# Optimization experiments

Hardware: AMD Instinct MI355X
Metric: run time of the kernel (lower is better)

## Reference

```python
import jax, jax.numpy as jnp
import numpy as np

D_MODEL = 1024
NUM_HEADS = 16
HEAD_DIM = D_MODEL // NUM_HEADS  # d_k = d_v = 64


def setup_inputs() -> dict:
    key = jax.random.key(0)
    ks = jax.random.split(key, 11)
    B, S = 2, 2048
    s = 1.0 / np.sqrt(D_MODEL)
    inp = {
        "query": jax.random.normal(ks[0], (B, S, D_MODEL), jnp.float32),
        "key": jax.random.normal(ks[1], (B, S, D_MODEL), jnp.float32),
        "value": jax.random.normal(ks[2], (B, S, D_MODEL), jnp.float32),
        "Wq": jax.random.normal(ks[3], (D_MODEL, D_MODEL), jnp.float32) * s,
        "bq": jax.random.normal(ks[4], (D_MODEL,), jnp.float32) * s,
        "Wk": jax.random.normal(ks[5], (D_MODEL, D_MODEL), jnp.float32) * s,
        "bk": jax.random.normal(ks[6], (D_MODEL,), jnp.float32) * s,
        "Wv": jax.random.normal(ks[7], (D_MODEL, D_MODEL), jnp.float32) * s,
        "bv": jax.random.normal(ks[8], (D_MODEL,), jnp.float32) * s,
        "Wo": jax.random.normal(ks[9], (D_MODEL, D_MODEL), jnp.float32) * s,
        "bo": jax.random.normal(ks[10], (D_MODEL,), jnp.float32) * s,
    }
    return inp


def reference(query, key, value, Wq, bq, Wk, bk, Wv, bv, Wo, bo):
    B, Sq, _ = query.shape
    # Linear projections (torch Linear: x @ W.T + b), split into heads
    def proj(x, W, b):
        y = x @ W.T + b  # [B, S, d_model]
        return y.reshape(B, -1, NUM_HEADS, HEAD_DIM).transpose(0, 2, 1, 3)  # [B, H, S, d]

    Q = proj(query, Wq, bq)
    K = proj(key, Wk, bk)
    V = proj(value, Wv, bv)

    scale = 1.0 / jnp.sqrt(jnp.asarray(HEAD_DIM, Q.dtype))
    scores = jnp.einsum("bhqd,bhkd->bhqk", Q, K) * scale  # [B, H, Sq, Sk]
    attn = jax.nn.softmax(scores, axis=-1)
    out = jnp.einsum("bhqk,bhkd->bhqd", attn, V)  # [B, H, Sq, d]
    out = out.transpose(0, 2, 1, 3).reshape(B, Sq, NUM_HEADS * HEAD_DIM)
    return out @ Wo.T + bo
```

## Files before the change

### kernel.cpp

```cpp
#include <hip/hip_runtime.h>
#include <hip/hip_bf16.h>

#define D_MODEL 1024
#define NHEADS  16
#define HDIM    64
#define BATCH   2
#define SEQ     2048
#define MTOT    (BATCH*SEQ)

typedef __attribute__((ext_vector_type(8))) short bf16x8;
typedef __attribute__((ext_vector_type(4))) float f32x4;

__device__ __forceinline__ void async_load16(const void* g, void* l) {
    __builtin_amdgcn_global_load_lds(
        (const __attribute__((address_space(1))) void*)g,
        (__attribute__((address_space(3))) void*)l, 16, 0, 0);
}

__device__ __forceinline__ short f2b(float x) {
    __hip_bfloat16 h = __float2bfloat16(x);
    return *reinterpret_cast<short*>(&h);
}
__device__ __forceinline__ unsigned pack2(float lo, float hi) {
    return (unsigned)(unsigned short)f2b(lo) | ((unsigned)(unsigned short)f2b(hi) << 16);
}

__global__ void cvt_all(const float* __restrict__ s0, const float* __restrict__ s1,
                        const float* __restrict__ s2, const float* __restrict__ s3,
                        const float* __restrict__ s4, const float* __restrict__ s5,
                        const float* __restrict__ s6,
                        short* __restrict__ d0, short* __restrict__ d1,
                        short* __restrict__ d2, short* __restrict__ d3,
                        short* __restrict__ d4, short* __restrict__ d5,
                        short* __restrict__ d6) {
    int bx = blockIdx.x;
    const float* src; short* dst; int blk;
    if (bx < 6144) {
        int t = bx >> 11; blk = bx & 2047;
        src = t == 0 ? s0 : (t == 1 ? s1 : s2);
        dst = t == 0 ? d0 : (t == 1 ? d1 : d2);
    } else {
        int t = (bx - 6144) >> 9; blk = (bx - 6144) & 511;
        src = t == 0 ? s3 : (t == 1 ? s4 : (t == 2 ? s5 : s6));
        dst = t == 0 ? d3 : (t == 1 ? d4 : (t == 2 ? d5 : d6));
    }
    int i = (blk * 256 + threadIdx.x) * 8;
    const float4* s4p = (const float4*)(src + i);
    float4 a = s4p[0], b = s4p[1];
    bf16x8 o;
    o[0]=f2b(a.x); o[1]=f2b(a.y); o[2]=f2b(a.z); o[3]=f2b(a.w);
    o[4]=f2b(b.x); o[5]=f2b(b.y); o[6]=f2b(b.z); o[7]=f2b(b.w);
    *(bf16x8*)(dst + i) = o;
}

__device__ __forceinline__ void gemm_core(const short* __restrict__ A,
                                          const short* __restrict__ Bt,
                                          int K, int m0, int n0,
                                          f32x4 (&acc)[4][4]) {
    __shared__ short As[128 * 32];
    __shared__ short Bs[128 * 32];
    const int lane = threadIdx.x & 63;
    const int wid  = threadIdx.x >> 6;
    const int wm   = (wid >> 1) * 64;
    const int wn   = (wid & 1) * 64;
    const int q    = lane & 15;
    const int quad = lane >> 4;
    const int lr   = lane >> 2;
    const int swzs = (lr + (lr >> 2)) & 3;
    const int cA   = (((lane & 3) ^ swzs)) * 8;
    const int kg   = (quad ^ ((q + (q >> 2)) & 3)) * 8;

#pragma unroll
    for (int mi = 0; mi < 4; mi++)
#pragma unroll
        for (int ni = 0; ni < 4; ni++)
            acc[mi][ni] = f32x4{0.f, 0.f, 0.f, 0.f};

    for (int k0 = 0; k0 < K; k0 += 32) {
#pragma unroll
        for (int c = 0; c < 2; ++c) {
            int chunk = wid * 2 + c;
            const short* ga = A  + (size_t)(m0 + chunk * 16 + lr) * K + k0 + cA;
            async_load16(ga, (char*)As + chunk * 1024);
            const short* gb = Bt + (size_t)(n0 + chunk * 16 + lr) * K + k0 + cA;
            async_load16(gb, (char*)Bs + chunk * 1024);
        }
        __syncthreads();
        bf16x8 af[4], bfr[4];
#pragma unroll
        for (int mi = 0; mi < 4; mi++)
            af[mi] = *(const bf16x8*)&As[(wm + mi * 16 + q) * 32 + kg];
#pragma unroll
        for (int ni = 0; ni < 4; ni++)
            bfr[ni] = *(const bf16x8*)&Bs[(wn + ni * 16 + q) * 32 + kg];
#pragma unroll
        for (int mi = 0; mi < 4; mi++)
#pragma unroll
            for (int ni = 0; ni < 4; ni++)
                acc[mi][ni] = __builtin_amdgcn_mfma_f32_16x16x32_bf16(
                    af[mi], bfr[ni], acc[mi][ni], 0, 0, 0);
        __syncthreads();
    }
}

#define QSCALE (0.125f * 1.44269504f)
__global__ __launch_bounds__(256) void proj_qkv(
    const short* __restrict__ xq, const short* __restrict__ xk, const short* __restrict__ xv,
    const short* __restrict__ wq, const short* __restrict__ wk, const short* __restrict__ wv,
    const float* __restrict__ bq, const float* __restrict__ bk, const float* __restrict__ bv,
    short* __restrict__ Qo, short* __restrict__ Ko, short* __restrict__ Vo) {
    const int z = blockIdx.z;
    const short* A    = z == 0 ? xq : (z == 1 ? xk : xv);
    const short* Bt   = z == 0 ? wq : (z == 1 ? wk : wv);
    const float* bias = z == 0 ? bq : (z == 1 ? bk : bv);
    short*       Out  = z == 0 ? Qo : (z == 1 ? Ko : Vo);
    const float scale = (z == 0) ? QSCALE : 1.0f;

    const int m0 = blockIdx.y * 128, n0 = blockIdx.x * 128;
    f32x4 acc[4][4];
    gemm_core(A, Bt, D_MODEL, m0, n0, acc);

    const int lane = threadIdx.x & 63;
    const int wid  = threadIdx.x >> 6;
    const int q = lane & 15, quad = lane >> 4;
    const int wm = (wid >> 1) * 64, wn = (wid & 1) * 64;
#pragma unroll
    for (int mi = 0; mi < 4; mi++)
#pragma unroll
        for (int ni = 0; ni < 4; ni++)
#pragma unroll
            for (int r = 0; r < 4; r++) {
                int m = m0 + wm + mi * 16 + quad * 4 + r;
                int n = n0 + wn + ni * 16 + q;
                float v = (acc[mi][ni][r] + bias[n]) * scale;
                int b = m >> 11, s = m & (SEQ - 1);
                int h = n >> 6, d = n & 63;
                Out[((size_t)(b * NHEADS + h) * SEQ + s) * HDIM + d] = f2b(v);
            }
}

__global__ __launch_bounds__(256) void gemm_out(
    const short* __restrict__ O, const short* __restrict__ wo,
    const float* __restrict__ bo, float* __restrict__ out) {
    const int m0 = blockIdx.y * 128, n0 = blockIdx.x * 128;
    f32x4 acc[4][4];
    gemm_core(O, wo, D_MODEL, m0, n0, acc);

    const int lane = threadIdx.x & 63;
    const int wid  = threadIdx.x >> 6;
    const int wm = (wid >> 1) * 64, wn = (wid & 1) * 64;
#pragma unroll
    for (int mi = 0; mi < 4; mi++)
#pragma unroll
        for (int ni = 0; ni < 4; ni++)
#pragma unroll
            for (int r = 0; r < 4; r++) {
                int m = m0 + wm + mi * 16 + (lane >> 4) * 4 + r;
                int n = n0 + wn + ni * 16 + (lane & 15);
                out[(size_t)m * D_MODEL + n] = acc[mi][ni][r] + bo[n];
            }
}

__global__ __launch_bounds__(256) void transpose_v(const short* __restrict__ Vp,
                                                   short* __restrict__ Vt) {
    const int bh = blockIdx.y, ts = blockIdx.x;
    __shared__ short T[64][72];
    const int tid = threadIdx.x;
    const int r = tid >> 2, c = (tid & 3) * 16;
    const bf16x8* g = (const bf16x8*)(Vp + ((size_t)bh * SEQ + ts * 64 + r) * HDIM + c);
    *(bf16x8*)&T[r][c]     = g[0];
    *(bf16x8*)&T[r][c + 8] = g[1];
    __syncthreads();
    bf16x8 o0, o1;
#pragma unroll
    for (int j = 0; j < 8; j++) o0[j] = T[c + j][r];
#pragma unroll
    for (int j = 0; j < 8; j++) o1[j] = T[c + 8 + j][r];
    short* dst = Vt + ((size_t)bh * HDIM + r) * SEQ + ts * 64 + c;
    *(bf16x8*)dst = o0;
    *(bf16x8*)(dst + 8) = o1;
}

#define C2 24.0f
__global__ __launch_bounds__(256, 2) void attn(
    const short* __restrict__ Q, const short* __restrict__ K,
    const short* __restrict__ Vt, short* __restrict__ O) {
    const int n = blockIdx.x;
    const int bh = ((n >> 8) << 3) | (n & 7);
    const int qb = (n >> 3) & 31;
    const int b = bh >> 4, h = bh & 15;
    const int q0 = qb * 64;
    const int lane = threadIdx.x & 63;
    const int w = threadIdx.x >> 6;
    const int q = lane & 15, quad = lane >> 4;
    const short* Qb  = Q + (size_t)bh * SEQ * HDIM;
    const short* Kb  = K + (size_t)bh * SEQ * HDIM;
    const short* Vtb = Vt + (size_t)bh * HDIM * SEQ;

    bf16x8 qf[4][2];
#pragma unroll
    for (int g = 0; g < 4; ++g)
#pragma unroll
        for (int c = 0; c < 2; ++c)
            qf[g][c] = *(const bf16x8*)(Qb + (size_t)(q0 + g * 16 + q) * HDIM +
                                        c * 32 + quad * 8);

    float lpart[4] = {0.f, 0.f, 0.f, 0.f};
    f32x4 oacc[4][4];
#pragma unroll
    for (int g = 0; g < 4; ++g)
#pragma unroll
        for (int dt = 0; dt < 4; dt++) oacc[g][dt] = f32x4{0.f, 0.f, 0.f, 0.f};

    const int s0l = ((quad & 1) << 5) | q;
    const int s1l = s0l + 16;

    for (int kt = w; kt < SEQ / 64; kt += 4) {
        const short* Kt = Kb + (size_t)kt * 64 * HDIM;
        bf16x8 kf[2][4], vf[2][4];
#pragma unroll
        for (int t = 0; t < 4; t++)
#pragma unroll
            for (int c = 0; c < 2; ++c)
                kf[c][t] = *(const bf16x8*)(Kt + (size_t)(t * 16 + q) * HDIM +
                                            c * 32 + quad * 8);
#pragma unroll
        for (int dt = 0; dt < 4; dt++)
#pragma unroll
            for (int c = 0; c < 2; ++c)
                vf[c][dt] = *(const bf16x8*)(Vtb + (size_t)(dt * 16 + q) * SEQ +
                                             kt * 64 + c * 32 + quad * 8);

#pragma unroll
        for (int g = 0; g < 4; ++g) {
            f32x4 st[4];
#pragma unroll
            for (int t = 0; t < 4; t++) {
                f32x4 s = f32x4{0.f, 0.f, 0.f, 0.f};
                s = __builtin_amdgcn_mfma_f32_16x16x32_bf16(kf[0][t], qf[g][0], s, 0, 0, 0);
                s = __builtin_amdgcn_mfma_f32_16x16x32_bf16(kf[1][t], qf[g][1], s, 0, 0, 0);
                st[t] = s;
            }
            float lp = lpart[g];
#pragma unroll
            for (int t = 0; t < 4; t++)
#pragma unroll
                for (int r = 0; r < 4; r++) {
                    float p = __builtin_amdgcn_exp2f(st[t][r] - C2);
                    st[t][r] = p;
                    lp += p;
                }
            lpart[g] = lp;
            unsigned pk[4][2];
#pragma unroll
            for (int t = 0; t < 4; t++) {
                pk[t][0] = pack2(st[t][0], st[t][1]);
                pk[t][1] = pack2(st[t][2], st[t][3]);
            }
            bf16x8 pb[2];
#pragma unroll
            for (int c = 0; c < 2; ++c) {
                unsigned lo0 = __shfl(pk[2 * c][0], s0l);
                unsigned lo1 = __shfl(pk[2 * c][1], s0l);
                unsigned lo2 = __shfl(pk[2 * c][0], s1l);
                unsigned lo3 = __shfl(pk[2 * c][1], s1l);
                unsigned hi0 = __shfl(pk[2 * c + 1][0], s0l);
                unsigned hi1 = __shfl(pk[2 * c + 1][1], s0l);
                unsigned hi2 = __shfl(pk[2 * c + 1][0], s1l);
                unsigned hi3 = __shfl(pk[2 * c + 1][1], s1l);
                uint4 u;
                u.x = quad < 2 ? lo0 : hi0;
                u.y = quad < 2 ? lo1 : hi1;
                u.z = quad < 2 ? lo2 : hi2;
                u.w = quad < 2 ? lo3 : hi3;
                pb[c] = __builtin_bit_cast(bf16x8, u);
            }
#pragma unroll
            for (int dt = 0; dt < 4; dt++) {
                oacc[g][dt] = __builtin_amdgcn_mfma_f32_16x16x32_bf16(vf[0][dt], pb[0],
                                                                     oacc[g][dt], 0, 0, 0);
                oacc[g][dt] = __builtin_amdgcn_mfma_f32_16x16x32_bf16(vf[1][dt], pb[1],
                                                                     oacc[g][dt], 0, 0, 0);
            }
        }
    }

    __shared__ f32x4 redO[4][4][64];
    __shared__ float redL[4][64];
#pragma unroll
    for (int g = 0; g < 4; ++g) {
        __syncthreads();
        redL[w][lane] = lpart[g];
#pragma unroll
        for (int dt = 0; dt < 4; dt++) redO[w][dt][lane] = oacc[g][dt];
        __syncthreads();
        float lt = 0.f;
#pragma unroll
        for (int w2 = 0; w2 < 4; ++w2)
#pragma unroll
            for (int qd = 0; qd < 4; ++qd) lt += redL[w2][qd * 16 + q];
        f32x4 o = redO[0][w][lane];
#pragma unroll
        for (int w2 = 1; w2 < 4; ++w2) {
            f32x4 t = redO[w2][w][lane];
#pragma unroll
            for (int r = 0; r < 4; r++) o[r] += t[r];
        }
        const float inv = 1.f / lt;
        const int qg = q0 + g * 16 + q;
        short* orow = O + ((size_t)(b * SEQ + qg)) * D_MODEL + h * HDIM;
        short4 s4;
        s4.x = f2b(o[0] * inv);
        s4.y = f2b(o[1] * inv);
        s4.z = f2b(o[2] * inv);
        s4.w = f2b(o[3] * inv);
        *(short4*)(orow + w * 16 + quad * 4) = s4;
    }
}

extern "C" void kernel_launch(void* const* d_in, const int* in_sizes, int n_in,
                              void* d_out, int out_size, void* d_ws, size_t ws_size,
                              hipStream_t stream) {
    (void)in_sizes; (void)n_in; (void)out_size; (void)ws_size;
    const float* q_in = (const float*)d_in[0];
    const float* k_in = (const float*)d_in[1];
    const float* v_in = (const float*)d_in[2];
    const float* Wq   = (const float*)d_in[3];
    const float* bq   = (const float*)d_in[4];
    const float* Wk   = (const float*)d_in[5];
    const float* bk   = (const float*)d_in[6];
    const float* Wv   = (const float*)d_in[7];
    const float* bv   = (const float*)d_in[8];
    const float* Wo   = (const float*)d_in[9];
    const float* bo   = (const float*)d_in[10];
    float* out = (float*)d_out;

    constexpr size_t MB = 1ull << 20;
    char* ws = (char*)d_ws;
    short* xq  = (short*)(ws + 0 * MB);
    short* xk  = (short*)(ws + 8 * MB);
    short* xv  = (short*)(ws + 16 * MB);
    short* wqb = (short*)(ws + 24 * MB);
    short* wkb = (short*)(ws + 26 * MB);
    short* wvb = (short*)(ws + 28 * MB);
    short* wob = (short*)(ws + 30 * MB);
    short* Qp  = (short*)(ws + 32 * MB);
    short* Kp  = (short*)(ws + 40 * MB);
    short* Vp  = (short*)(ws + 48 * MB);
    short* Op  = (short*)(ws + 56 * MB);
    short* VtG = (short*)(ws + 0 * MB);

    cvt_all<<<8192, 256, 0, stream>>>(q_in, k_in, v_in, Wq, Wk, Wv, Wo,
                                      xq, xk, xv, wqb, wkb, wvb, wob);
    proj_qkv<<<dim3(8, 32, 3), 256, 0, stream>>>(xq, xk, xv, wqb, wkb, wvb,
                                                 bq, bk, bv, Qp, Kp, Vp);
    transpose_v<<<dim3(SEQ / 64, BATCH * NHEADS), 256, 0, stream>>>(Vp, VtG);
    attn<<<1024, 256, 0, stream>>>(Qp, Kp, VtG, Op);
    gemm_out<<<dim3(8, 32), 256, 0, stream>>>(Op, wob, bo, out);
}
```

Before: 254.6 us.

## Split attention waves across query and key halves; use bit-trick bf16 conversion

The attention kernel now handles 128 queries per block. Two wave pairs each cover 64 queries and split the key tiles between them, which halves the grid and the cross-wave reduction traffic per output. Each K/V tile is reused by two query groups per block, but each wave walks twice as many key tiles, and with fewer blocks there may be fewer waves to hide latency. Separately, the float-to-bf16 conversion becomes an add-and-shift round-half-up bit trick with a perm pack instead of the library conversion, which drops round-to-nearest-even and NaN handling.

```diff
diff --git a/kernel.cpp b/kernel.cpp
--- a/kernel.cpp
+++ b/kernel.cpp
@@ -18,11 +18,13 @@
 }
 
 __device__ __forceinline__ short f2b(float x) {
-    __hip_bfloat16 h = __float2bfloat16(x);
-    return *reinterpret_cast<short*>(&h);
+    unsigned u = __builtin_bit_cast(unsigned, x) + 0x8000u;
+    return (short)(u >> 16);
 }
 __device__ __forceinline__ unsigned pack2(float lo, float hi) {
-    return (unsigned)(unsigned short)f2b(lo) | ((unsigned)(unsigned short)f2b(hi) << 16);
+    unsigned ulo = __builtin_bit_cast(unsigned, lo) + 0x8000u;
+    unsigned uhi = __builtin_bit_cast(unsigned, hi) + 0x8000u;
+    return __builtin_amdgcn_perm(uhi, ulo, 0x07060302u);
 }
 
 __global__ void cvt_all(const float* __restrict__ s0, const float* __restrict__ s1,
@@ -47,10 +49,10 @@
     int i = (blk * 256 + threadIdx.x) * 8;
     const float4* s4p = (const float4*)(src + i);
     float4 a = s4p[0], b = s4p[1];
-    bf16x8 o;
-    o[0]=f2b(a.x); o[1]=f2b(a.y); o[2]=f2b(a.z); o[3]=f2b(a.w);
-    o[4]=f2b(b.x); o[5]=f2b(b.y); o[6]=f2b(b.z); o[7]=f2b(b.w);
-    *(bf16x8*)(dst + i) = o;
+    unsigned u0 = pack2(a.x, a.y), u1 = pack2(a.z, a.w);
+    unsigned u2 = pack2(b.x, b.y), u3 = pack2(b.z, b.w);
+    uint4 o; o.x = u0; o.y = u1; o.z = u2; o.w = u3;
+    *(uint4*)(dst + i) = o;
 }
 
 __device__ __forceinline__ void gemm_core(const short* __restrict__ A,
@@ -186,12 +188,13 @@
     const short* __restrict__ Q, const short* __restrict__ K,
     const short* __restrict__ Vt, short* __restrict__ O) {
     const int n = blockIdx.x;
-    const int bh = ((n >> 8) << 3) | (n & 7);
-    const int qb = (n >> 3) & 31;
+    const int bh = ((n >> 7) << 3) | (n & 7);
+    const int qb = (n >> 3) & 15;
     const int b = bh >> 4, h = bh & 15;
-    const int q0 = qb * 64;
     const int lane = threadIdx.x & 63;
     const int w = threadIdx.x >> 6;
+    const int wq = w & 1, wk = w >> 1;
+    const int q0 = qb * 128 + wq * 64;
     const int q = lane & 15, quad = lane >> 4;
     const short* Qb  = Q + (size_t)bh * SEQ * HDIM;
     const short* Kb  = K + (size_t)bh * SEQ * HDIM;
@@ -215,7 +218,7 @@
     const int s0l = ((quad & 1) << 5) | q;
     const int s1l = s0l + 16;
 
-    for (int kt = w; kt < SEQ / 64; kt += 4) {
+    for (int kt = wk; kt < SEQ / 64; kt += 2) {
         const short* Kt = Kb + (size_t)kt * 64 * HDIM;
         bf16x8 kf[2][4], vf[2][4];
 #pragma unroll
@@ -296,25 +299,26 @@
         __syncthreads();
         float lt = 0.f;
 #pragma unroll
-        for (int w2 = 0; w2 < 4; ++w2)
-#pragma unroll
-            for (int qd = 0; qd < 4; ++qd) lt += redL[w2][qd * 16 + q];
-        f32x4 o = redO[0][w][lane];
-#pragma unroll
-        for (int w2 = 1; w2 < 4; ++w2) {
-            f32x4 t = redO[w2][w][lane];
-#pragma unroll
-            for (int r = 0; r < 4; r++) o[r] += t[r];
-        }
+        for (int wk2 = 0; wk2 < 2; ++wk2)
+#pragma unroll
+            for (int qd = 0; qd < 4; ++qd) lt += redL[wq + wk2 * 2][qd * 16 + q];
         const float inv = 1.f / lt;
         const int qg = q0 + g * 16 + q;
         short* orow = O + ((size_t)(b * SEQ + qg)) * D_MODEL + h * HDIM;
-        short4 s4;
-        s4.x = f2b(o[0] * inv);
-        s4.y = f2b(o[1] * inv);
-        s4.z = f2b(o[2] * inv);
-        s4.w = f2b(o[3] * inv);
-        *(short4*)(orow + w * 16 + quad * 4) = s4;
+#pragma unroll
+        for (int dd = 0; dd < 2; ++dd) {
+            const int dt = wk * 2 + dd;
+            f32x4 o = redO[wq][dt][lane];
+            f32x4 t2 = redO[wq + 2][dt][lane];
+#pragma unroll
+            for (int r = 0; r < 4; r++) o[r] += t2[r];
+            short4 s4;
+            s4.x = f2b(o[0] * inv);
+            s4.y = f2b(o[1] * inv);
+            s4.z = f2b(o[2] * inv);
+            s4.w = f2b(o[3] * inv);
+            *(short4*)(orow + dt * 16 + quad * 4) = s4;
+        }
     }
 }
 
@@ -355,6 +359,6 @@
     proj_qkv<<<dim3(8, 32, 3), 256, 0, stream>>>(xq, xk, xv, wqb, wkb, wvb,
                                                  bq, bk, bv, Qp, Kp, Vp);
     transpose_v<<<dim3(SEQ / 64, BATCH * NHEADS), 256, 0, stream>>>(Vp, VtG);
-    attn<<<1024, 256, 0, stream>>>(Qp, Kp, VtG, Op);
+    attn<<<512, 256, 0, stream>>>(Qp, Kp, VtG, Op);
     gemm_out<<<dim3(8, 32), 256, 0, stream>>>(Op, wob, bo, out);
 }
```

Measured after the change: 251.3 us. No clear change (-1.3%).
